# Kernel tuning notes

Hardware: AMD Instinct MI355X
Metric: run time of the kernel (lower is better)

The kernel has to match this reference:

```python
import jax, jax.numpy as jnp
import numpy as np

B, T, D, H = 2, 2048, 2048, 16
HD = D // H  # head_dim = 128
NEG = -1e9


def setup_inputs() -> dict:
    key = jax.random.key(0)
    k1, k2, k3 = jax.random.split(key, 3)
    x = jax.random.normal(k1, (B, T, D), dtype=jnp.float32)
    # additive causal mask: 0 on/below diagonal, large negative above
    mask = jnp.where(jnp.tril(jnp.ones((T, T), dtype=bool)), 0.0, NEG).astype(jnp.float32)
    causal_mask = mask[None, None]  # [1,1,T,T]
    w_qkv = jax.random.normal(k2, (3 * D, D), dtype=jnp.float32) * (D ** -0.5)
    w_out = jax.random.normal(k3, (D, D), dtype=jnp.float32) * (D ** -0.5)
    b_out = jnp.zeros((D,), dtype=jnp.float32)
    return {"x": x, "causal_mask": causal_mask, "w_qkv": w_qkv, "w_out": w_out, "b_out": b_out}


def reference(x, causal_mask, w_qkv, w_out, b_out):
    scale = HD ** -0.5
    qkv = jnp.einsum('btd,ed->bte', x, w_qkv)          # [B,T,3D]
    q, k, v = jnp.split(qkv, 3, axis=-1)
    def heads(t):  # [B,T,D] -> [B,H,T,HD]
        return t.reshape(B, T, H, HD).transpose(0, 2, 1, 3)
    q, k, v = heads(q), heads(k), heads(v)
    attn = jnp.einsum('bhqd,bhkd->bhqk', q, k) * scale + causal_mask
    attn = jax.nn.softmax(attn, axis=-1)
    out = jnp.einsum('bhqk,bhkd->bhqd', attn, v)       # [B,H,T,HD]
    out = out.transpose(0, 2, 1, 3).reshape(B, T, D)
    return jnp.einsum('btd,ed->bte', out, w_out) + b_out
```

## Files before the change

kernel.cpp:

```cpp
#include <hip/hip_runtime.h>
#include <stdint.h>

typedef uint16_t u16;
typedef __attribute__((ext_vector_type(8))) short short8;
typedef __attribute__((ext_vector_type(4))) float f32x4;
typedef __attribute__((ext_vector_type(16))) float f32x16;

#define MFMA16(a, b, c) __builtin_amdgcn_mfma_f32_16x16x32_bf16((a), (b), (c), 0, 0, 0)
#define MFMA32(a, b, c) __builtin_amdgcn_mfma_f32_32x32x16_bf16((a), (b), (c), 0, 0, 0)
#define AS1 __attribute__((address_space(1)))
#define AS3 __attribute__((address_space(3)))

__device__ __forceinline__ void gld_lds16(const u16* g, u16* l) {
  __builtin_amdgcn_global_load_lds((const AS1 void*)g, (AS3 void*)l, 16, 0, 0);
}

__device__ __forceinline__ u16 f2bf(float f) {
  uint32_t u = __float_as_uint(f);
  u += 0x7fffu + ((u >> 16) & 1u);
  return (u16)(u >> 16);
}

__global__ __launch_bounds__(256) void cvt_all(const float* __restrict__ x,
                                               const float* __restrict__ wqkv,
                                               const float* __restrict__ wout,
                                               u16* __restrict__ xb,
                                               u16* __restrict__ wqkvb,
                                               u16* __restrict__ woutb) {
  const int n1 = 8388608 / 4, n2 = 12582912 / 4;
  int i = blockIdx.x * 256 + threadIdx.x;
  const float* src;
  u16* dst;
  int j;
  if (i < n1) {
    src = x; dst = xb; j = i;
  } else if (i < n1 + n2) {
    src = wqkv; dst = wqkvb; j = i - n1;
  } else {
    src = wout; dst = woutb; j = i - n1 - n2;
  }
  float4 v = ((const float4*)src)[j];
  uint2 o;
  o.x = (uint32_t)f2bf(v.x) | ((uint32_t)f2bf(v.y) << 16);
  o.y = (uint32_t)f2bf(v.z) | ((uint32_t)f2bf(v.w) << 16);
  ((uint2*)dst)[j] = o;
}

template <int N>
__device__ __forceinline__ void bar_vm() {
  asm volatile("s_waitcnt vmcnt(%0)\n\ts_barrier" ::"n"(N) : "memory");
}

template <int MFR>
__device__ __forceinline__ void gemm_core3(const u16* __restrict__ Ab,
                                           const u16* __restrict__ Bb,
                                           u16* sm, int tid,
                                           f32x4 acc[MFR][4]) {
  constexpr int AROWS = MFR * 32;
  constexpr int ASZ = AROWS * 32;
  constexpr int BSZ = 128 * 32;
  constexpr int BUF = ASZ + BSZ;
  constexpr int NT = 64;
  constexpr int ALD = AROWS / 64;
  constexpr int VN = ALD + 2;
  const int lane = tid & 63, w = tid >> 6;
  const int wr = w >> 1, wc = w & 1;
  const int lo = lane & 15, q4 = lane >> 4;
  const int ch = (q4 + 4 - (lo >> 2)) & 3;

  auto stage = [&](int g) {
    u16* As = sm + (g % 3) * BUF;
    u16* Bs = As + ASZ;
    const int k0 = g * 32;
#pragma unroll
    for (int s = 0; s < ALD; ++s) {
      const int c = tid + s * 256;
      const int row = c >> 2, cc = c & 3;
      const int cs = (cc + (row >> 2)) & 3;
      gld_lds16(Ab + (size_t)row * 2048 + k0 + cs * 8, As + c * 8);
    }
#pragma unroll
    for (int s = 0; s < 2; ++s) {
      const int c = tid + s * 256;
      const int row = c >> 2, cc = c & 3;
      const int cs = (cc + (row >> 2)) & 3;
      gld_lds16(Bb + (size_t)row * 2048 + k0 + cs * 8, Bs + c * 8);
    }
  };

  stage(0);
  stage(1);
  bar_vm<VN>();

  for (int g = 0; g < NT; ++g) {
    const u16* As = sm + (g % 3) * BUF;
    const u16* Bs = As + ASZ;
    if (g + 2 < NT) stage(g + 2);
    short8 af[MFR], bf[4];
#pragma unroll
    for (int i = 0; i < MFR; ++i)
      af[i] = *(const short8*)(As + (wr * (MFR * 16) + i * 16 + lo) * 32 + ch * 8);
#pragma unroll
    for (int j = 0; j < 4; ++j)
      bf[j] = *(const short8*)(Bs + (wc * 64 + j * 16 + lo) * 32 + ch * 8);
    __builtin_amdgcn_s_setprio(1);
#pragma unroll
    for (int i = 0; i < MFR; ++i)
#pragma unroll
      for (int j = 0; j < 4; ++j) acc[i][j] = MFMA16(af[i], bf[j], acc[i][j]);
    __builtin_amdgcn_s_setprio(0);
    if (g + 1 < NT) {
      if (g + 2 < NT) {
        bar_vm<VN>();
      } else {
        bar_vm<0>();
      }
    }
  }
}

__global__ __launch_bounds__(256, 2) void proj_gemm(const u16* __restrict__ xb,
                                                    const u16* __restrict__ wqkvb,
                                                    u16* __restrict__ qkb,
                                                    u16* __restrict__ vtb) {
  __shared__ u16 sm[3 * (256 * 32 + 128 * 32)];
  int bx = blockIdx.x;
  bx = (bx & 7) * 96 + (bx >> 3);
  const int tid = threadIdx.x;
  const u16 *Ab, *Bb;
  u16* C;
  if (bx < 512) {
    const int mt = bx >> 5, nt = bx & 31;
    Ab = xb + (size_t)mt * 256 * 2048;
    Bb = wqkvb + (size_t)nt * 128 * 2048;
    C = qkb + (size_t)mt * 256 * 4096 + nt * 128;
  } else {
    const int idx = bx - 512, mt = idx >> 5, nt = idx & 31;
    Ab = wqkvb + (size_t)(4096 + mt * 256) * 2048;
    Bb = xb + (size_t)nt * 128 * 2048;
    C = vtb + (size_t)mt * 256 * 4096 + nt * 128;
  }
  f32x4 acc[8][4];
  const f32x4 fzero = {0.f, 0.f, 0.f, 0.f};
#pragma unroll
  for (int i = 0; i < 8; ++i)
#pragma unroll
    for (int j = 0; j < 4; ++j) acc[i][j] = fzero;

  gemm_core3<8>(Ab, Bb, sm, tid, acc);

  const int lane = tid & 63, w = tid >> 6;
  const int wr = w >> 1, wc = w & 1;
  const int lo = lane & 15, q4 = lane >> 4;
#pragma unroll
  for (int i = 0; i < 8; ++i)
#pragma unroll
    for (int j = 0; j < 4; ++j) {
      const int col = wc * 64 + j * 16 + lo;
#pragma unroll
      for (int e = 0; e < 4; ++e) {
        const int row = wr * 128 + i * 16 + q4 * 4 + e;
        C[(size_t)row * 4096 + col] = f2bf(acc[i][j][e]);
      }
    }
}

__global__ __launch_bounds__(256, 2) void out_gemm(const u16* __restrict__ A,
                                                   const u16* __restrict__ B,
                                                   float* __restrict__ Cf,
                                                   const float* __restrict__ bias) {
  __shared__ u16 sm[3 * (128 * 32 + 128 * 32)];
  int bx = blockIdx.x;
  bx = (bx & 7) * 64 + (bx >> 3);
  const int tid = threadIdx.x;
  const int mt = bx >> 4, nt = bx & 15;
  const u16* Ab = A + (size_t)mt * 128 * 2048;
  const u16* Bb = B + (size_t)nt * 128 * 2048;
  f32x4 acc[4][4];
  const f32x4 fzero = {0.f, 0.f, 0.f, 0.f};
#pragma unroll
  for (int i = 0; i < 4; ++i)
#pragma unroll
    for (int j = 0; j < 4; ++j) acc[i][j] = fzero;

  gemm_core3<4>(Ab, Bb, sm, tid, acc);

  const int lane = tid & 63, w = tid >> 6;
  const int wr = w >> 1, wc = w & 1;
  const int lo = lane & 15, q4 = lane >> 4;
#pragma unroll
  for (int i = 0; i < 4; ++i)
#pragma unroll
    for (int j = 0; j < 4; ++j) {
      const int col = nt * 128 + wc * 64 + j * 16 + lo;
      const float bv = bias[col];
#pragma unroll
      for (int e = 0; e < 4; ++e) {
        const int row = mt * 128 + wr * 64 + i * 16 + q4 * 4 + e;
        Cf[(size_t)row * 2048 + col] = acc[i][j][e] + bv;
      }
    }
}

__device__ __forceinline__ int swz(int r, int c) {
  return r * 128 + (c ^ (((r ^ (r >> 3)) & 7) << 4));
}

__global__ __launch_bounds__(512) void flash_attn(const u16* __restrict__ qk,
                                                  const u16* __restrict__ vt,
                                                  u16* __restrict__ aout) {
  constexpr int T = 2048, WQK = 4096, D = 2048;
  constexpr int TILE = 128 * 128;
  __shared__ u16 smem[5 * TILE];

  const int bx = blockIdx.x;
  const int p = bx >> 5;
  const int g = bx & 31;
  const int h = g & 15, b = g >> 4;
  const int tid = threadIdx.x, lane = tid & 63, w = tid >> 6;
  const int wr = w >> 1, wcc = w & 1;
  const int l31 = lane & 31, h5 = lane >> 5;

  const u16* Qb = qk + (size_t)b * T * WQK + h * 128;
  const u16* Kb = Qb + 2048;
  const u16* Vtb = vt + (size_t)h * 128 * 4096 + b * 2048;
  u16* Ps = smem + 4 * TILE;

  const float cexp = 0.08838834764831843f * 1.4426950408889634f;
  short8 onesf;
#pragma unroll
  for (int j = 0; j < 8; ++j) onesf[j] = (short)0x3F80;

  for (int half = 0; half < 2; ++half) {
    const int qt = half ? p : 15 - p;
    const int q0 = qt * 128;

    short8 qf[8];
#pragma unroll
    for (int kc = 0; kc < 8; ++kc)
      qf[kc] = *(const short8*)(Qb + (size_t)(q0 + wr * 32 + l31) * WQK +
                                kc * 16 + h5 * 8);

    f32x16 o[2], osum;
#pragma unroll
    for (int e = 0; e < 16; ++e) { o[0][e] = 0.f; o[1][e] = 0.f; osum[e] = 0.f; }

    __syncthreads();
#pragma unroll
    for (int s = 0; s < 4; ++s) {
      const int c = tid + s * 512, r = c >> 4, cc = c & 15;
      const int cs = cc ^ (((r ^ (r >> 3)) & 7) << 1);
      gld_lds16(Kb + (size_t)r * WQK + cs * 8, smem + c * 8);
      gld_lds16(Vtb + (size_t)r * 4096 + cs * 8, smem + 2 * TILE + c * 8);
    }

    for (int kt = 0; kt <= qt; ++kt) {
      const int curo = (kt & 1) * TILE, nxto = TILE - curo;
      __syncthreads();
      if (kt < qt) {
        const int k0n = (kt + 1) * 128;
#pragma unroll
        for (int s = 0; s < 4; ++s) {
          const int c = tid + s * 512, r = c >> 4, cc = c & 15;
          const int cs = cc ^ (((r ^ (r >> 3)) & 7) << 1);
          gld_lds16(Kb + (size_t)(k0n + r) * WQK + cs * 8, smem + nxto + c * 8);
          gld_lds16(Vtb + (size_t)r * 4096 + k0n + cs * 8,
                    smem + 2 * TILE + nxto + c * 8);
        }
      }

      const u16* Ksc = smem + curo;
      const u16* Vsc = smem + 2 * TILE + curo;

      f32x16 s2[2];
#pragma unroll
      for (int e = 0; e < 16; ++e) { s2[0][e] = 0.f; s2[1][e] = 0.f; }
#pragma unroll
      for (int kc = 0; kc < 8; ++kc)
#pragma unroll
        for (int ct = 0; ct < 2; ++ct) {
          short8 kf = *(const short8*)&Ksc[swz(wcc * 64 + ct * 32 + l31,
                                               kc * 16 + h5 * 8)];
          s2[ct] = MFMA32(qf[kc], kf, s2[ct]);
        }

      const bool diag = (kt == qt);
#pragma unroll
      for (int ct = 0; ct < 2; ++ct) {
        const int kcol = wcc * 64 + ct * 32 + l31;
#pragma unroll
        for (int reg = 0; reg < 16; ++reg) {
          const int qrow = wr * 32 + (reg & 3) + 8 * (reg >> 2) + 4 * h5;
          float pv = exp2f(s2[ct][reg] * cexp);
          if (diag && (kcol > qrow)) pv = 0.f;
          Ps[swz(qrow, kcol)] = f2bf(pv);
        }
      }
      asm volatile("s_waitcnt lgkmcnt(0)\n\ts_barrier" ::: "memory");

#pragma unroll
      for (int kc = 0; kc < 8; ++kc) {
        short8 pa = *(const short8*)&Ps[swz(wr * 32 + l31, kc * 16 + h5 * 8)];
        osum = MFMA32(pa, onesf, osum);
#pragma unroll
        for (int dt = 0; dt < 2; ++dt) {
          short8 vf = *(const short8*)&Vsc[swz(wcc * 64 + dt * 32 + l31,
                                               kc * 16 + h5 * 8)];
          o[dt] = MFMA32(pa, vf, o[dt]);
        }
      }
    }

#pragma unroll
    for (int reg = 0; reg < 16; ++reg) {
      const int row = q0 + wr * 32 + (reg & 3) + 8 * (reg >> 2) + 4 * h5;
      const float inv = 1.f / osum[reg];
#pragma unroll
      for (int dt = 0; dt < 2; ++dt)
        aout[(size_t)(b * T + row) * D + h * 128 + wcc * 64 + dt * 32 + l31] =
            f2bf(o[dt][reg] * inv);
    }
  }
}

extern "C" void kernel_launch(void* const* d_in, const int* in_sizes, int n_in,
                              void* d_out, int out_size, void* d_ws, size_t ws_size,
                              hipStream_t stream) {
  const float* x = (const float*)d_in[0];
  const float* w_qkv = (const float*)d_in[2];
  const float* w_out = (const float*)d_in[3];
  const float* b_out = (const float*)d_in[4];
  float* out = (float*)d_out;

  const int BT = 4096, D = 2048, D3 = 6144;
  u16* xb = (u16*)d_ws;
  u16* wqkvb = xb + (size_t)BT * D;
  u16* woutb = wqkvb + (size_t)D3 * D;
  u16* qkb = woutb + (size_t)D * D;
  u16* vtb = qkb + (size_t)BT * 4096;
  u16* attnb = vtb + (size_t)D * BT;

  const int total4 = (BT * D + D3 * D + D * D) / 4;
  cvt_all<<<total4 / 256, 256, 0, stream>>>(x, w_qkv, w_out, xb, wqkvb, woutb);
  proj_gemm<<<768, 256, 0, stream>>>(xb, wqkvb, qkb, vtb);
  flash_attn<<<256, 512, 0, stream>>>(qkb, vtb, attnb);
  out_gemm<<<512, 256, 0, stream>>>(attnb, woutb, out, b_out);
}
```

Before: 357.6 us.

## Rework GEMM LDS swizzle and rebalance projection and output GEMM tiling

Changes the LDS layout in the shared GEMM core to an XOR swizzle that packs two rows per 64-element line, so MFMA fragment reads avoid bank conflicts. The projection GEMM now splits the V^T part into 128x128 tiles (1024 blocks instead of 768), which balances work across CUs. The output GEMM moves to 256x128 tiles with 256 blocks to raise reuse per block. The larger tiles use more registers and LDS and leave fewer blocks in flight for the output GEMM.

```diff
diff --git a/kernel.cpp b/kernel.cpp
--- a/kernel.cpp
+++ b/kernel.cpp
@@ -63,10 +63,12 @@
   constexpr int NT = 64;
   constexpr int ALD = AROWS / 64;
   constexpr int VN = ALD + 2;
+
   const int lane = tid & 63, w = tid >> 6;
   const int wr = w >> 1, wc = w & 1;
   const int lo = lane & 15, q4 = lane >> 4;
-  const int ch = (q4 + 4 - (lo >> 2)) & 3;
+  const int pcl = (((lo & 1) << 2) | q4) ^ ((lo >> 1) & 7);
+  const int loff = (lo >> 1) * 64 + pcl * 8;
 
   auto stage = [&](int g) {
     u16* As = sm + (g % 3) * BUF;
@@ -75,16 +77,18 @@
 #pragma unroll
     for (int s = 0; s < ALD; ++s) {
       const int c = tid + s * 256;
-      const int row = c >> 2, cc = c & 3;
-      const int cs = (cc + (row >> 2)) & 3;
-      gld_lds16(Ab + (size_t)row * 2048 + k0 + cs * 8, As + c * 8);
+      const int sr = c >> 3, pc = c & 7;
+      const int t = pc ^ (sr & 7);
+      const int r = sr * 2 + (t >> 2), c4 = t & 3;
+      gld_lds16(Ab + (size_t)r * 2048 + k0 + c4 * 8, As + c * 8);
     }
 #pragma unroll
     for (int s = 0; s < 2; ++s) {
       const int c = tid + s * 256;
-      const int row = c >> 2, cc = c & 3;
-      const int cs = (cc + (row >> 2)) & 3;
-      gld_lds16(Bb + (size_t)row * 2048 + k0 + cs * 8, Bs + c * 8);
+      const int sr = c >> 3, pc = c & 7;
+      const int t = pc ^ (sr & 7);
+      const int r = sr * 2 + (t >> 2), c4 = t & 3;
+      gld_lds16(Bb + (size_t)r * 2048 + k0 + c4 * 8, Bs + c * 8);
     }
   };
 
@@ -99,10 +103,10 @@
     short8 af[MFR], bf[4];
 #pragma unroll
     for (int i = 0; i < MFR; ++i)
-      af[i] = *(const short8*)(As + (wr * (MFR * 16) + i * 16 + lo) * 32 + ch * 8);
+      af[i] = *(const short8*)(As + (wr * (MFR * 16) + i * 16) * 32 + loff);
 #pragma unroll
     for (int j = 0; j < 4; ++j)
-      bf[j] = *(const short8*)(Bs + (wc * 64 + j * 16 + lo) * 32 + ch * 8);
+      bf[j] = *(const short8*)(Bs + (wc * 64 + j * 16) * 32 + loff);
     __builtin_amdgcn_s_setprio(1);
 #pragma unroll
     for (int i = 0; i < MFR; ++i)
@@ -124,79 +128,96 @@
                                                     u16* __restrict__ qkb,
                                                     u16* __restrict__ vtb) {
   __shared__ u16 sm[3 * (256 * 32 + 128 * 32)];
-  int bx = blockIdx.x;
-  bx = (bx & 7) * 96 + (bx >> 3);
   const int tid = threadIdx.x;
-  const u16 *Ab, *Bb;
-  u16* C;
-  if (bx < 512) {
-    const int mt = bx >> 5, nt = bx & 31;
-    Ab = xb + (size_t)mt * 256 * 2048;
-    Bb = wqkvb + (size_t)nt * 128 * 2048;
-    C = qkb + (size_t)mt * 256 * 4096 + nt * 128;
-  } else {
-    const int idx = bx - 512, mt = idx >> 5, nt = idx & 31;
-    Ab = wqkvb + (size_t)(4096 + mt * 256) * 2048;
-    Bb = xb + (size_t)nt * 128 * 2048;
-    C = vtb + (size_t)mt * 256 * 4096 + nt * 128;
-  }
-  f32x4 acc[8][4];
-  const f32x4 fzero = {0.f, 0.f, 0.f, 0.f};
-#pragma unroll
-  for (int i = 0; i < 8; ++i)
-#pragma unroll
-    for (int j = 0; j < 4; ++j) acc[i][j] = fzero;
-
-  gemm_core3<8>(Ab, Bb, sm, tid, acc);
-
   const int lane = tid & 63, w = tid >> 6;
   const int wr = w >> 1, wc = w & 1;
   const int lo = lane & 15, q4 = lane >> 4;
-#pragma unroll
-  for (int i = 0; i < 8; ++i)
-#pragma unroll
-    for (int j = 0; j < 4; ++j) {
-      const int col = wc * 64 + j * 16 + lo;
-#pragma unroll
-      for (int e = 0; e < 4; ++e) {
-        const int row = wr * 128 + i * 16 + q4 * 4 + e;
-        C[(size_t)row * 4096 + col] = f2bf(acc[i][j][e]);
-      }
-    }
+
+  if (blockIdx.x < 512) {
+    int bx = blockIdx.x;
+    bx = (bx & 7) * 64 + (bx >> 3);
+    const int mt = bx >> 5, nt = bx & 31;
+    const u16* Ab = xb + (size_t)mt * 256 * 2048;
+    const u16* Bb = wqkvb + (size_t)nt * 128 * 2048;
+    u16* C = qkb + (size_t)mt * 256 * 4096 + nt * 128;
+    f32x4 acc[8][4];
+    const f32x4 fzero = {0.f, 0.f, 0.f, 0.f};
+#pragma unroll
+    for (int i = 0; i < 8; ++i)
+#pragma unroll
+      for (int j = 0; j < 4; ++j) acc[i][j] = fzero;
+    gemm_core3<8>(Ab, Bb, sm, tid, acc);
+#pragma unroll
+    for (int i = 0; i < 8; ++i)
+#pragma unroll
+      for (int j = 0; j < 4; ++j) {
+        const int col = wc * 64 + j * 16 + lo;
+#pragma unroll
+        for (int e = 0; e < 4; ++e) {
+          const int row = wr * 128 + i * 16 + q4 * 4 + e;
+          C[(size_t)row * 4096 + col] = f2bf(acc[i][j][e]);
+        }
+      }
+  } else {
+    int idx = blockIdx.x - 512;
+    idx = (idx & 7) * 64 + (idx >> 3);
+    const int mt = idx >> 5, nt = idx & 31;
+    const u16* Ab = wqkvb + (size_t)(4096 + mt * 128) * 2048;
+    const u16* Bb = xb + (size_t)nt * 128 * 2048;
+    u16* C = vtb + (size_t)mt * 128 * 4096 + nt * 128;
+    f32x4 acc[4][4];
+    const f32x4 fzero = {0.f, 0.f, 0.f, 0.f};
+#pragma unroll
+    for (int i = 0; i < 4; ++i)
+#pragma unroll
+      for (int j = 0; j < 4; ++j) acc[i][j] = fzero;
+    gemm_core3<4>(Ab, Bb, sm, tid, acc);
+#pragma unroll
+    for (int i = 0; i < 4; ++i)
+#pragma unroll
+      for (int j = 0; j < 4; ++j) {
+        const int col = wc * 64 + j * 16 + lo;
+#pragma unroll
+        for (int e = 0; e < 4; ++e) {
+          const int row = wr * 64 + i * 16 + q4 * 4 + e;
+          C[(size_t)row * 4096 + col] = f2bf(acc[i][j][e]);
+        }
+      }
+  }
 }
 
 __global__ __launch_bounds__(256, 2) void out_gemm(const u16* __restrict__ A,
                                                    const u16* __restrict__ B,
                                                    float* __restrict__ Cf,
                                                    const float* __restrict__ bias) {
-  __shared__ u16 sm[3 * (128 * 32 + 128 * 32)];
+  __shared__ u16 sm[3 * (256 * 32 + 128 * 32)];
   int bx = blockIdx.x;
-  bx = (bx & 7) * 64 + (bx >> 3);
+  bx = (bx & 7) * 32 + (bx >> 3);
   const int tid = threadIdx.x;
   const int mt = bx >> 4, nt = bx & 15;
-  const u16* Ab = A + (size_t)mt * 128 * 2048;
+  const u16* Ab = A + (size_t)mt * 256 * 2048;
   const u16* Bb = B + (size_t)nt * 128 * 2048;
-  f32x4 acc[4][4];
+  f32x4 acc[8][4];
   const f32x4 fzero = {0.f, 0.f, 0.f, 0.f};
 #pragma unroll
-  for (int i = 0; i < 4; ++i)
+  for (int i = 0; i < 8; ++i)
 #pragma unroll
     for (int j = 0; j < 4; ++j) acc[i][j] = fzero;
 
-  gemm_core3<4>(Ab, Bb, sm, tid, acc);
+  gemm_core3<8>(Ab, Bb, sm, tid, acc);
 
   const int lane = tid & 63, w = tid >> 6;
   const int wr = w >> 1, wc = w & 1;
   const int lo = lane & 15, q4 = lane >> 4;
 #pragma unroll
-  for (int i = 0; i < 4; ++i)
+  for (int i = 0; i < 8; ++i)
 #pragma unroll
     for (int j = 0; j < 4; ++j) {
       const int col = nt * 128 + wc * 64 + j * 16 + lo;
       const float bv = bias[col];
 #pragma unroll
       for (int e = 0; e < 4; ++e) {
-        const int row = mt * 128 + wr * 64 + i * 16 + q4 * 4 + e;
+        const int row = mt * 256 + wr * 128 + i * 16 + q4 * 4 + e;
         Cf[(size_t)row * 2048 + col] = acc[i][j][e] + bv;
       }
     }
@@ -342,7 +363,7 @@
 
   const int total4 = (BT * D + D3 * D + D * D) / 4;
   cvt_all<<<total4 / 256, 256, 0, stream>>>(x, w_qkv, w_out, xb, wqkvb, woutb);
-  proj_gemm<<<768, 256, 0, stream>>>(xb, wqkvb, qkb, vtb);
+  proj_gemm<<<1024, 256, 0, stream>>>(xb, wqkvb, qkb, vtb);
   flash_attn<<<256, 512, 0, stream>>>(qkb, vtb, attnb);
-  out_gemm<<<512, 256, 0, stream>>>(attnb, woutb, out, b_out);
-}
+  out_gemm<<<256, 256, 0, stream>>>(attnb, woutb, out, b_out);
+}
```

After: 366.4 us. 1.02x slower.
